# Kernel optimization log

Hardware: AMD Instinct MI355X
Metric: run time of the kernel (lower is better)

The kernel has to match this reference:

```python
import jax, jax.numpy as jnp
import numpy as np
from jax import lax

B, C, H, W = 16, 64, 256, 256
EPS = 1e-5


def conv2d(x, w, b, pad):
    # x: [B,Cin,H,W], w: [Cout,Cin,kh,kw]
    out = lax.conv_general_dilated(x, w, (1, 1), [(pad, pad), (pad, pad)],
                                   dimension_numbers=("NCHW", "OIHW", "NCHW"))
    return out + b[None, :, None, None]


def setup_inputs() -> dict:
    key = jax.random.key(0)
    ks = jax.random.split(key, 12)
    s = 0.05
    return {
        "x": jax.random.normal(ks[0], (B, C, H, W), jnp.float32),
        "conv_w": jax.random.normal(ks[1], (C, C, 3, 3), jnp.float32) * s,
        "conv_b": jax.random.normal(ks[2], (C,), jnp.float32) * s,
        "bn_gamma": jnp.ones((C,), jnp.float32),
        "bn_beta": jnp.zeros((C,), jnp.float32),
        "bn_mean": jax.random.normal(ks[3], (C,), jnp.float32) * s,
        "bn_var": jax.random.uniform(ks[4], (C,), jnp.float32, 0.5, 1.5),
        "attn_w": jax.random.normal(ks[5], (1, C, 1, 1), jnp.float32) * s,
        "attn_b": jax.random.normal(ks[6], (1,), jnp.float32) * s,
        "dir1_w": jax.random.normal(ks[7], (8, C, 1, 1), jnp.float32) * s,
        "dir1_b": jax.random.normal(ks[8], (8,), jnp.float32) * s,
        "dir2_w": jax.random.normal(ks[9], (1, 8, 1, 1), jnp.float32) * s,
        "dir2_b": jax.random.normal(ks[10], (1,), jnp.float32) * s,
    }


def reference(x, conv_w, conv_b, bn_gamma, bn_beta, bn_mean, bn_var,
              attn_w, attn_b, dir1_w, dir1_b, dir2_w, dir2_b):
    # conv -> BN (eval) -> ReLU
    feat = conv2d(x, conv_w, conv_b, pad=1)
    feat = (feat - bn_mean[None, :, None, None]) * (
        bn_gamma[None, :, None, None] * lax.rsqrt(bn_var + EPS)[None, :, None, None]
    ) + bn_beta[None, :, None, None]
    feat = jax.nn.relu(feat)

    # direction branch: global avg pool -> 1x1 conv -> relu -> 1x1 conv -> sigmoid
    pooled = jnp.mean(x, axis=(2, 3))                      # [B,C]
    h1 = jax.nn.relu(pooled @ dir1_w[:, :, 0, 0].T + dir1_b)  # [B,8]
    direction = jax.nn.sigmoid(h1 @ dir2_w[:, :, 0, 0].T + dir2_b)  # [B,1]
    direction = direction[:, :, None, None]                # [B,1,1,1]

    # attention map [B,1,H,W]
    att = jnp.einsum("bchw,oc->bohw", feat, attn_w[:, :, 0, 0]) + attn_b[None, :, None, None]

    # trapezoid mask: per-row weight depending on direction > 0.5
    j = jnp.arange(H, dtype=x.dtype) / H                   # [H]
    w_up = 0.5 + 0.5 * j
    w_dn = 1.0 - 0.5 * j
    cond = direction[:, 0, 0, 0] > 0.5                     # [B]
    mask = jnp.where(cond[:, None], w_up[None, :], w_dn[None, :])  # [B,H]
    mask = mask[:, None, :, None]                          # [B,1,H,1]

    att = jax.nn.sigmoid(att * mask)
    return x * att, direction
```

## Files before the change

### kernel.cpp

```cpp
#include <hip/hip_runtime.h>
#include <hip/hip_bf16.h>

typedef __attribute__((ext_vector_type(8))) short  s8v;
typedef __attribute__((ext_vector_type(4))) float  f4v;
typedef __attribute__((ext_vector_type(4))) unsigned short u4v;

#define XH 256
#define XW 256
#define PLANE 65536
#define PCW 66

__device__ __forceinline__ unsigned short f2bf(float f){
  __hip_bfloat16 h = __float2bfloat16(f);
  return __builtin_bit_cast(unsigned short, h);
}
__device__ __forceinline__ float bf2f(unsigned short h){
  unsigned int u = ((unsigned int)h) << 16;
  return __builtin_bit_cast(float, u);
}

__global__ __launch_bounds__(256) void pool_k(const float* __restrict__ x,
                                              float* __restrict__ pooled){
  int plane = blockIdx.x, t = threadIdx.x;
  const f4v* p = (const f4v*)(x + (size_t)plane * PLANE);
  float s = 0.f;
  #pragma unroll 8
  for(int it = 0; it < 64; ++it){
    f4v v = p[t + (it << 8)];
    s += v[0] + v[1] + v[2] + v[3];
  }
  #pragma unroll
  for(int m = 32; m >= 1; m >>= 1) s += __shfl_xor(s, m);
  __shared__ float ps[4];
  if((t & 63) == 0) ps[t >> 6] = s;
  __syncthreads();
  if(t == 0) pooled[plane] = (ps[0] + ps[1] + ps[2] + ps[3]) * (1.f / 65536.f);
}

__global__ __launch_bounds__(256) void prep_k(const float* __restrict__ convw,
    const float* __restrict__ convb, const float* __restrict__ gamma,
    const float* __restrict__ beta,  const float* __restrict__ mean,
    const float* __restrict__ var,   const float* __restrict__ d1w,
    const float* __restrict__ d1b,   const float* __restrict__ d2w,
    const float* __restrict__ d2b,   const float* __restrict__ pooled,
    float* __restrict__ dirv, float* __restrict__ bias2,
    unsigned short* __restrict__ pk, float* __restrict__ outdir){
  int blk = blockIdx.x, t = threadIdx.x;
  if(blk == 0){
    __shared__ float h1s[16][8];
    if(t < 128){
      int b = t >> 3, o = t & 7;
      float a = d1b[o];
      #pragma unroll 8
      for(int c = 0; c < 64; ++c) a = fmaf(pooled[b * 64 + c], d1w[o * 64 + c], a);
      h1s[b][o] = fmaxf(a, 0.f);
    } else if(t >= 128 && t < 192){
      int oc = t - 128;
      float sc = gamma[oc] * rsqrtf(var[oc] + 1e-5f);
      bias2[oc] = (convb[oc] - mean[oc]) * sc + beta[oc];
    }
    __syncthreads();
    if(t < 16){
      float logit = d2b[0];
      #pragma unroll
      for(int o = 0; o < 8; ++o) logit = fmaf(h1s[t][o], d2w[o], logit);
      float dv = 1.f / (1.f + __expf(-logit));
      dirv[t] = dv;
      outdir[t] = dv;
    }
  } else {
    int idx = ((blk - 1) << 8) + t;
    int j = idx & 7, g = (idx >> 3) & 3, n = (idx >> 5) & 63, s = idx >> 11;
    int c = ((s & 1) << 5) + (g << 3) + j, tap = s >> 1;
    float sc = gamma[n] * rsqrtf(var[n] + 1e-5f);
    pk[idx] = f2bf(convw[(n * 64 + c) * 9 + tap] * sc);
  }
}

__global__ __launch_bounds__(256, 3) void main_k(const float* __restrict__ x,
    const float* __restrict__ attnw, const float* __restrict__ attnb,
    const float* __restrict__ dirv,  const float* __restrict__ bias2,
    const unsigned short* __restrict__ pk, float* __restrict__ out){
  __shared__ __align__(16) char lds[6 * PCW * 128 + 4 * 64 * 4];
  float* att_s = (float*)(lds + 6 * PCW * 128);

  const int bid = blockIdx.x;
  const int bs  = ((bid & 7) << 9) | (bid >> 3);
  const int wblk = bs & 3, hblk = (bs >> 2) & 63, b = bs >> 8;
  const int w0 = wblk << 6, h0 = hblk << 2;
  const int t = threadIdx.x, lane = t & 63, wv = t >> 6;
  const int lm = lane & 15, lg = lane >> 4;
  const size_t bbase = (size_t)b * 64 * PLANE;

  const char* pkl = (const char*)pk + lm * 64 + (lg << 4);

#define BLOAD(BUF, S) { \
    _Pragma("unroll") \
    for(int jn = 0; jn < 4; ++jn) BUF[jn] = *(const s8v*)(pkl + ((S) << 12) + (jn << 10)); }

  s8v bb0[4], bb1[4], bb2[4];
  BLOAD(bb0, 0); BLOAD(bb1, 1); BLOAD(bb2, 2);

  #pragma unroll 2
  for(int it = 0; it < 7; ++it){
    int task = t + (it << 8);
    if(task < 1728){
      int chunk = task % 18;
      int rem   = task / 18;
      int hh = rem % 6, cgrp = rem / 6;
      int hhg = h0 - 1 + hh;
      int wcg = w0 - 4 + (chunk << 2);
      f4v v0 = {0,0,0,0}, v1 = {0,0,0,0}, v2 = {0,0,0,0}, v3 = {0,0,0,0};
      if(hhg >= 0 && hhg < XH && wcg >= 0 && wcg + 3 < XW){
        const float* bp = x + bbase + (size_t)(cgrp << 2) * PLANE + (size_t)hhg * XW + wcg;
        v0 = *(const f4v*)bp;
        v1 = *(const f4v*)(bp + PLANE);
        v2 = *(const f4v*)(bp + 2 * PLANE);
        v3 = *(const f4v*)(bp + 3 * PLANE);
      }
      #pragma unroll
      for(int e = 0; e < 4; ++e){
        int pc = (chunk << 2) - 3 + e;
        if(pc >= 0 && pc < PCW){
          int pix = hh * PCW + pc;
          int s16 = (cgrp >> 1) ^ ((pix >> 2) & 7);
          int bo  = pix * 128 + (s16 << 4) + ((cgrp & 1) << 3);
          unsigned long long d =
              (unsigned long long)f2bf(v0[e])
            | ((unsigned long long)f2bf(v1[e]) << 16)
            | ((unsigned long long)f2bf(v2[e]) << 32)
            | ((unsigned long long)f2bf(v3[e]) << 48);
          *(unsigned long long*)(lds + bo) = d;
        }
      }
    }
  }
  __syncthreads();

  f4v acc[4][4];
  #pragma unroll
  for(int i = 0; i < 4; ++i)
    #pragma unroll
    for(int j = 0; j < 4; ++j) acc[i][j] = (f4v){0.f, 0.f, 0.f, 0.f};

  const int pixb = (wv + 1) * PCW + lm + 1;

#define ALOAD(AFR, D, SCH) { \
    _Pragma("unroll") \
    for(int i = 0; i < 4; ++i){ int pix = pixb + (i << 4) + (D); \
      int sl = ((SCH) ^ ((pix >> 2) & 7)) << 4; \
      AFR[i] = *(const s8v*)(lds + pix * 128 + sl); } }
#define MF(AFR, BUF) { \
    _Pragma("unroll") \
    for(int i = 0; i < 4; ++i){ _Pragma("unroll") for(int j = 0; j < 4; ++j) \
      acc[i][j] = __builtin_amdgcn_mfma_f32_16x16x32_bf16(AFR[i], BUF[j], acc[i][j], 0, 0, 0); } }
#define STEPX(S, BUF) { \
    s8v afr[4]; \
    const int dd = (((S) >> 1) / 3 - 1) * PCW + (((S) >> 1) % 3 - 1); \
    ALOAD(afr, dd, lg + (((S) & 1) << 2)); \
    __builtin_amdgcn_s_setprio(1); \
    MF(afr, BUF); \
    __builtin_amdgcn_s_setprio(0); \
    if((S) + 3 < 18) BLOAD(BUF, (S) + 3); }

  STEPX(0,  bb0) STEPX(1,  bb1) STEPX(2,  bb2)
  STEPX(3,  bb0) STEPX(4,  bb1) STEPX(5,  bb2)
  STEPX(6,  bb0) STEPX(7,  bb1) STEPX(8,  bb2)
  STEPX(9,  bb0) STEPX(10, bb1) STEPX(11, bb2)
  STEPX(12, bb0) STEPX(13, bb1) STEPX(14, bb2)
  STEPX(15, bb0) STEPX(16, bb1) STEPX(17, bb2)

  float aw[4], bz[4];
  #pragma unroll
  for(int j = 0; j < 4; ++j){ aw[j] = attnw[(j << 4) + lm]; bz[j] = bias2[(j << 4) + lm]; }
  #pragma unroll
  for(int i = 0; i < 4; ++i){
    #pragma unroll
    for(int r = 0; r < 4; ++r){
      float lsum = 0.f;
      #pragma unroll
      for(int j = 0; j < 4; ++j)
        lsum = fmaf(aw[j], fmaxf(acc[i][j][r] + bz[j], 0.f), lsum);
      lsum += __shfl_xor(lsum, 8);
      lsum += __shfl_xor(lsum, 4);
      lsum += __shfl_xor(lsum, 2);
      lsum += __shfl_xor(lsum, 1);
      if(lm == (i << 2) + r) att_s[(wv << 6) + (i << 4) + (lg << 2) + r] = lsum;
    }
  }
  __syncthreads();

  const int col = lane, row = wv;
  const float dir = dirv[b];
  const int h = h0 + row;
  const float jf = (float)h * (1.f / 256.f);
  const float maskv = (dir > 0.5f) ? (0.5f + 0.5f * jf) : (1.f - 0.5f * jf);
  const float att = att_s[(row << 6) + col] + attnb[0];
  const float sg = 1.f / (1.f + __expf(-att * maskv));
  const int pix = (row + 1) * PCW + (col + 1);
  const char* xr = lds + pix * 128;
  const int pq = (pix >> 2) & 7;
  float* op = out + bbase + (size_t)h * XW + w0 + col;
  #pragma unroll
  for(int k = 0; k < 8; ++k){
    s8v v = *(const s8v*)(xr + ((k ^ pq) << 4));
    #pragma unroll
    for(int e = 0; e < 8; ++e){
      op[(size_t)((k << 3) + e) * PLANE] = bf2f((unsigned short)v[e]) * sg;
    }
  }
#undef ALOAD
#undef BLOAD
#undef MF
#undef STEPX
}

extern "C" void kernel_launch(void* const* d_in, const int* in_sizes, int n_in,
                              void* d_out, int out_size, void* d_ws, size_t ws_size,
                              hipStream_t stream){
  const float* x     = (const float*)d_in[0];
  const float* convw = (const float*)d_in[1];
  const float* convb = (const float*)d_in[2];
  const float* gamma = (const float*)d_in[3];
  const float* beta  = (const float*)d_in[4];
  const float* mean  = (const float*)d_in[5];
  const float* var   = (const float*)d_in[6];
  const float* attnw = (const float*)d_in[7];
  const float* attnb = (const float*)d_in[8];
  const float* d1w   = (const float*)d_in[9];
  const float* d1b   = (const float*)d_in[10];
  const float* d2w   = (const float*)d_in[11];
  const float* d2b   = (const float*)d_in[12];
  float* out = (float*)d_out;
  char*  ws  = (char*)d_ws;
  float* pooled = (float*)ws;
  float* dirv   = (float*)(ws + 4096);
  float* bias2  = (float*)(ws + 4352);
  unsigned short* pk = (unsigned short*)(ws + 5120);
  float* outdir = out + (size_t)16 * 64 * 256 * 256;

  pool_k<<<1024, 256, 0, stream>>>(x, pooled);
  prep_k<<<145, 256, 0, stream>>>(convw, convb, gamma, beta, mean, var,
                                  d1w, d1b, d2w, d2b, pooled, dirv, bias2, pk, outdir);
  main_k<<<4096, 256, 0, stream>>>(x, attnw, attnb, dirv, bias2, pk, out);
}
```

Baseline: 601.3 us.

## Stage input channels in two halves to halve LDS and raise occupancy

The conv input tile is now staged into LDS in two 32-channel halves, and the K-steps are reordered so each half is consumed before the next is loaded. This halves the LDS footprint, and the launch bound is raised from 3 to 6 blocks per CU. The final multiply now re-reads x from global memory in fp32 with vectorized float4 loads and stores, replacing the bf16 copy in LDS, which also restores full precision in the output. The sigmoid is folded into the reduction step, in exchange for extra global reads of x and an extra barrier between the halves.

```diff
diff --git a/kernel.cpp b/kernel.cpp
--- a/kernel.cpp
+++ b/kernel.cpp
@@ -3,7 +3,8 @@
 
 typedef __attribute__((ext_vector_type(8))) short  s8v;
 typedef __attribute__((ext_vector_type(4))) float  f4v;
-typedef __attribute__((ext_vector_type(4))) unsigned short u4v;
+typedef __attribute__((ext_vector_type(2))) unsigned long long ull2;
+typedef unsigned long long ull;
 
 #define XH 256
 #define XW 256
@@ -77,12 +78,12 @@
   }
 }
 
-__global__ __launch_bounds__(256, 3) void main_k(const float* __restrict__ x,
+__global__ __launch_bounds__(256, 6) void main_k(const float* __restrict__ x,
     const float* __restrict__ attnw, const float* __restrict__ attnb,
     const float* __restrict__ dirv,  const float* __restrict__ bias2,
     const unsigned short* __restrict__ pk, float* __restrict__ out){
-  __shared__ __align__(16) char lds[6 * PCW * 128 + 4 * 64 * 4];
-  float* att_s = (float*)(lds + 6 * PCW * 128);
+  __shared__ __align__(16) char lds[6 * PCW * 64];
+  __shared__ __align__(16) float att_s[256];
 
   const int bid = blockIdx.x;
   const int bs  = ((bid & 7) << 9) | (bid >> 3);
@@ -99,43 +100,34 @@
     for(int jn = 0; jn < 4; ++jn) BUF[jn] = *(const s8v*)(pkl + ((S) << 12) + (jn << 10)); }
 
   s8v bb0[4], bb1[4], bb2[4];
-  BLOAD(bb0, 0); BLOAD(bb1, 1); BLOAD(bb2, 2);
-
-  #pragma unroll 2
-  for(int it = 0; it < 7; ++it){
-    int task = t + (it << 8);
-    if(task < 1728){
-      int chunk = task % 18;
-      int rem   = task / 18;
-      int hh = rem % 6, cgrp = rem / 6;
-      int hhg = h0 - 1 + hh;
-      int wcg = w0 - 4 + (chunk << 2);
-      f4v v0 = {0,0,0,0}, v1 = {0,0,0,0}, v2 = {0,0,0,0}, v3 = {0,0,0,0};
-      if(hhg >= 0 && hhg < XH && wcg >= 0 && wcg + 3 < XW){
-        const float* bp = x + bbase + (size_t)(cgrp << 2) * PLANE + (size_t)hhg * XW + wcg;
-        v0 = *(const f4v*)bp;
-        v1 = *(const f4v*)(bp + PLANE);
-        v2 = *(const f4v*)(bp + 2 * PLANE);
-        v3 = *(const f4v*)(bp + 3 * PLANE);
-      }
-      #pragma unroll
-      for(int e = 0; e < 4; ++e){
-        int pc = (chunk << 2) - 3 + e;
-        if(pc >= 0 && pc < PCW){
-          int pix = hh * PCW + pc;
-          int s16 = (cgrp >> 1) ^ ((pix >> 2) & 7);
-          int bo  = pix * 128 + (s16 << 4) + ((cgrp & 1) << 3);
-          unsigned long long d =
-              (unsigned long long)f2bf(v0[e])
-            | ((unsigned long long)f2bf(v1[e]) << 16)
-            | ((unsigned long long)f2bf(v2[e]) << 32)
-            | ((unsigned long long)f2bf(v3[e]) << 48);
-          *(unsigned long long*)(lds + bo) = d;
-        }
-      }
-    }
-  }
-  __syncthreads();
+  BLOAD(bb0, 0); BLOAD(bb1, 2); BLOAD(bb2, 4);
+
+#define STAGE(P) { \
+    _Pragma("unroll") \
+    for(int it = 0; it < 4; ++it){ \
+      int task = t + (it << 8); \
+      if(task < 864){                       \
+        int chunk = task % 18; int rem = task / 18; \
+        int hh = rem % 6, cg = rem / 6; \
+        int hhg = h0 - 1 + hh; \
+        int wcg = w0 - 4 + (chunk << 2); \
+        f4v v0 = {0,0,0,0}, v1 = {0,0,0,0}, v2 = {0,0,0,0}, v3 = {0,0,0,0}; \
+        if(hhg >= 0 && hhg < XH && wcg >= 0 && wcg + 3 < XW){ \
+          const float* bp = x + bbase + (size_t)(((((P) << 3) + cg)) << 2) * PLANE \
+                              + (size_t)hhg * XW + wcg; \
+          v0 = *(const f4v*)bp;             v1 = *(const f4v*)(bp + PLANE); \
+          v2 = *(const f4v*)(bp + 2*PLANE); v3 = *(const f4v*)(bp + 3*PLANE); \
+        } \
+        _Pragma("unroll") \
+        for(int e = 0; e < 4; ++e){ \
+          int pc = (chunk << 2) - 3 + e; \
+          if(pc >= 0 && pc < PCW){ \
+            int pix = hh * PCW + pc; \
+            int s8 = cg ^ ((pix >> 2) & 7); \
+            ull d = (ull)f2bf(v0[e]) | ((ull)f2bf(v1[e]) << 16) \
+                  | ((ull)f2bf(v2[e]) << 32) | ((ull)f2bf(v3[e]) << 48); \
+            *(ull*)(lds + pix * 64 + (s8 << 3)) = d; \
+          } } } } }
 
   f4v acc[4][4];
   #pragma unroll
@@ -145,34 +137,47 @@
 
   const int pixb = (wv + 1) * PCW + lm + 1;
 
-#define ALOAD(AFR, D, SCH) { \
-    _Pragma("unroll") \
-    for(int i = 0; i < 4; ++i){ int pix = pixb + (i << 4) + (D); \
-      int sl = ((SCH) ^ ((pix >> 2) & 7)) << 4; \
-      AFR[i] = *(const s8v*)(lds + pix * 128 + sl); } }
+#define ALOAD(AFR, D) { \
+    _Pragma("unroll") \
+    for(int i = 0; i < 4; ++i){ \
+      int pix = pixb + (i << 4) + (D); \
+      int pq = (pix >> 2) & 7; \
+      ull2 tv; \
+      tv[0] = *(const ull*)(lds + pix * 64 + ((((lg << 1)    ) ^ pq) << 3)); \
+      tv[1] = *(const ull*)(lds + pix * 64 + ((((lg << 1) | 1) ^ pq) << 3)); \
+      AFR[i] = __builtin_bit_cast(s8v, tv); } }
 #define MF(AFR, BUF) { \
     _Pragma("unroll") \
     for(int i = 0; i < 4; ++i){ _Pragma("unroll") for(int j = 0; j < 4; ++j) \
       acc[i][j] = __builtin_amdgcn_mfma_f32_16x16x32_bf16(AFR[i], BUF[j], acc[i][j], 0, 0, 0); } }
-#define STEPX(S, BUF) { \
+#define STEPP(S, BUF, NS) { \
     s8v afr[4]; \
-    const int dd = (((S) >> 1) / 3 - 1) * PCW + (((S) >> 1) % 3 - 1); \
-    ALOAD(afr, dd, lg + (((S) & 1) << 2)); \
+    const int dd = ((((S) >> 1) / 3) - 1) * PCW + (((S) >> 1) % 3) - 1; \
+    ALOAD(afr, dd); \
     __builtin_amdgcn_s_setprio(1); \
     MF(afr, BUF); \
     __builtin_amdgcn_s_setprio(0); \
-    if((S) + 3 < 18) BLOAD(BUF, (S) + 3); }
-
-  STEPX(0,  bb0) STEPX(1,  bb1) STEPX(2,  bb2)
-  STEPX(3,  bb0) STEPX(4,  bb1) STEPX(5,  bb2)
-  STEPX(6,  bb0) STEPX(7,  bb1) STEPX(8,  bb2)
-  STEPX(9,  bb0) STEPX(10, bb1) STEPX(11, bb2)
-  STEPX(12, bb0) STEPX(13, bb1) STEPX(14, bb2)
-  STEPX(15, bb0) STEPX(16, bb1) STEPX(17, bb2)
+    if((NS) >= 0) BLOAD(BUF, NS); }
+
+  STAGE(0)
+  __syncthreads();
+  STEPP(0,  bb0, 6)  STEPP(2,  bb1, 8)  STEPP(4,  bb2, 10)
+  STEPP(6,  bb0, 12) STEPP(8,  bb1, 14) STEPP(10, bb2, 16)
+  STEPP(12, bb0, 1)  STEPP(14, bb1, 3)  STEPP(16, bb2, 5)
+  __syncthreads();
+  STAGE(1)
+  __syncthreads();
+  STEPP(1,  bb0, 7)  STEPP(3,  bb1, 9)  STEPP(5,  bb2, 11)
+  STEPP(7,  bb0, 13) STEPP(9,  bb1, 15) STEPP(11, bb2, 17)
+  STEPP(13, bb0, -1) STEPP(15, bb1, -1) STEPP(17, bb2, -1)
 
   float aw[4], bz[4];
   #pragma unroll
   for(int j = 0; j < 4; ++j){ aw[j] = attnw[(j << 4) + lm]; bz[j] = bias2[(j << 4) + lm]; }
+  const float dir = dirv[b];
+  const float jf = (float)(h0 + wv) * (1.f / 256.f);
+  const float maskv = (dir > 0.5f) ? (0.5f + 0.5f * jf) : (1.f - 0.5f * jf);
+  const float ab = attnb[0];
   #pragma unroll
   for(int i = 0; i < 4; ++i){
     #pragma unroll
@@ -185,34 +190,33 @@
       lsum += __shfl_xor(lsum, 4);
       lsum += __shfl_xor(lsum, 2);
       lsum += __shfl_xor(lsum, 1);
-      if(lm == (i << 2) + r) att_s[(wv << 6) + (i << 4) + (lg << 2) + r] = lsum;
+      if(lm == (i << 2) + r){
+        float sg = 1.f / (1.f + __expf(-(lsum + ab) * maskv));
+        att_s[(wv << 6) + (i << 4) + (lg << 2) + r] = sg;
+      }
     }
   }
   __syncthreads();
 
-  const int col = lane, row = wv;
-  const float dir = dirv[b];
-  const int h = h0 + row;
-  const float jf = (float)h * (1.f / 256.f);
-  const float maskv = (dir > 0.5f) ? (0.5f + 0.5f * jf) : (1.f - 0.5f * jf);
-  const float att = att_s[(row << 6) + col] + attnb[0];
-  const float sg = 1.f / (1.f + __expf(-att * maskv));
-  const int pix = (row + 1) * PCW + (col + 1);
-  const char* xr = lds + pix * 128;
-  const int pq = (pix >> 2) & 7;
-  float* op = out + bbase + (size_t)h * XW + w0 + col;
-  #pragma unroll
-  for(int k = 0; k < 8; ++k){
-    s8v v = *(const s8v*)(xr + ((k ^ pq) << 4));
-    #pragma unroll
-    for(int e = 0; e < 8; ++e){
-      op[(size_t)((k << 3) + e) * PLANE] = bf2f((unsigned short)v[e]) * sg;
-    }
+  const int wq = t & 15, cb = t >> 4;
+  #pragma unroll
+  for(int k = 0; k < 16; ++k){
+    const int ch  = cb + ((k & 3) << 4);
+    const int row = k >> 2;
+    const size_t off = bbase + (size_t)ch * PLANE + (size_t)(h0 + row) * XW
+                     + w0 + (wq << 2);
+    f4v xv = *(const f4v*)(x + off);
+    f4v av = *(const f4v*)(att_s + (row << 6) + (wq << 2));
+    f4v o;
+    o[0] = xv[0] * av[0]; o[1] = xv[1] * av[1];
+    o[2] = xv[2] * av[2]; o[3] = xv[3] * av[3];
+    *(f4v*)(out + off) = o;
   }
 #undef ALOAD
 #undef BLOAD
 #undef MF
-#undef STEPX
+#undef STEPP
+#undef STAGE
 }
 
 extern "C" void kernel_launch(void* const* d_in, const int* in_sizes, int n_in,
```

Result: slower. 2.222 ms (+269.6%).
